# Optimization experiments

Hardware: AMD Instinct MI355X
Metric: run time of the kernel (lower is better)

Reference implementation:

```python
import jax, jax.numpy as jnp
import numpy as np

NUM_GROUPS = 32
EPS = 1e-5
HEAD_DIM = 64

def group_norm(x, w, b):
    # x: [B,C,H,W]; normalize within 32 groups over (C//32, H, W)
    B, C, H, W = x.shape
    xg = x.reshape(B, NUM_GROUPS, C // NUM_GROUPS, H, W)
    mu = xg.mean(axis=(2, 3, 4), keepdims=True)
    var = xg.var(axis=(2, 3, 4), keepdims=True)
    xn = ((xg - mu) / jnp.sqrt(var + EPS)).reshape(B, C, H, W)
    return xn * w[None, :, None, None] + b[None, :, None, None]

def conv1x1(x, w, b):
    # w: [Cout, Cin], b: [Cout]
    return jnp.einsum('bchw,oc->bohw', x, w) + b[None, :, None, None]

def setup_inputs() -> dict:
    key = jax.random.key(0)
    ks = jax.random.split(key, 12)
    B, C, Cc, H, W = 16, 512, 512, 32, 32
    s = 0.02
    return {
        'x': jax.random.normal(ks[0], (B, C, H, W), jnp.float32),
        'context': jax.random.normal(ks[1], (B, Cc, H, W), jnp.float32),
        'norm_q_w': jnp.ones((C,), jnp.float32),
        'norm_q_b': jnp.zeros((C,), jnp.float32),
        'norm_kv_w': jnp.ones((Cc,), jnp.float32),
        'norm_kv_b': jnp.zeros((Cc,), jnp.float32),
        'conv_q_w': jax.random.normal(ks[2], (C, C), jnp.float32) * s,
        'conv_q_b': jnp.zeros((C,), jnp.float32),
        'conv_kv_w': jax.random.normal(ks[3], (2 * C, Cc), jnp.float32) * s,
        'conv_kv_b': jnp.zeros((2 * C,), jnp.float32),
        'proj_w': jax.random.normal(ks[4], (C, C), jnp.float32) * s,
        'proj_b': jnp.zeros((C,), jnp.float32),
    }

def reference(x, context, norm_q_w, norm_q_b, norm_kv_w, norm_kv_b,
              conv_q_w, conv_q_b, conv_kv_w, conv_kv_b, proj_w, proj_b):
    B, C, H, W = x.shape
    nh = max(1, C // HEAD_DIM)
    hd = C // nh
    q = conv1x1(group_norm(x, norm_q_w, norm_q_b), conv_q_w, conv_q_b)
    kv = conv1x1(group_norm(context, norm_kv_w, norm_kv_b), conv_kv_w, conv_kv_b)
    k, v = jnp.split(kv, 2, axis=1)
    L = H * W
    q = q.reshape(B, nh, hd, L)
    k = k.reshape(B, nh, hd, L)
    v = v.reshape(B, nh, hd, L)
    attn = jnp.einsum('bhdi,bhdj->bhij', q, k) * (hd ** -0.5)
    attn = jax.nn.softmax(attn, axis=-1)
    out = jnp.einsum('bhij,bhdj->bhdi', attn, v)
    return x + conv1x1(out.reshape(B, C, H, W), proj_w, proj_b)
```

## Files before the change

### kernel.cpp

```cpp
#include <hip/hip_runtime.h>
#include <hip/hip_bf16.h>

typedef short v8s __attribute__((ext_vector_type(8)));
typedef float v4f __attribute__((ext_vector_type(4)));
typedef float v16f __attribute__((ext_vector_type(16)));
typedef __hip_bfloat16 bf16;

__device__ __forceinline__ float b2f(bf16 h) { return __bfloat162float(h); }
__device__ __forceinline__ bf16 f2b(float f) { return __float2bfloat16(f); }

#define QSCALE 0.18033688f

__device__ __forceinline__ void gll16(const void* g, void* l) {
    __builtin_amdgcn_global_load_lds(
        (const __attribute__((address_space(1))) void*)g,
        (__attribute__((address_space(3))) void*)l, 16, 0, 0);
}

__device__ __forceinline__ unsigned cvtpk(float lo, float hi_) {
    unsigned r;
    asm("v_cvt_pk_bf16_f32 %0, %1, %2" : "=v"(r) : "v"(lo), "v"(hi_));
    return r;
}

__device__ __forceinline__ void pl32swap(unsigned& a, unsigned& b) {
    asm("v_permlane32_swap_b32 %0, %1" : "+v"(a), "+v"(b));
}

__global__ __launch_bounds__(256) void gn_t_kernel(
    const float* __restrict__ x, const float* __restrict__ ctx,
    const float* __restrict__ qw, const float* __restrict__ qb,
    const float* __restrict__ kw, const float* __restrict__ kb,
    bf16* __restrict__ xnT, bf16* __restrict__ cnT)
{
    const int b = blockIdx.y, g = blockIdx.x, z = blockIdx.z, c0 = g * 16;
    const float* src = z ? ctx : x;
    const float* gw  = z ? kw : qw;
    const float* gb  = z ? kb : qb;
    bf16* dst = z ? cnT : xnT;
    __shared__ __attribute__((aligned(16))) bf16 lx[16][1032];
    __shared__ float rS[4], rQ[4];
    __shared__ float sSc[16], sSh[16];
    const int t = threadIdx.x, wave = t >> 6, lane = t & 63;
    const float* xb = src + ((long)b * 512 + c0) * 1024;
    float sum = 0.f, sq = 0.f;
#pragma unroll
    for (int i = 0; i < 16; i++) {
        int q = t + i * 256;
        int ci = q >> 8, l0 = (q & 255) * 4;
        float4 v = *(const float4*)(xb + (long)ci * 1024 + l0);
        sum += v.x + v.y + v.z + v.w;
        sq  += v.x * v.x + v.y * v.y + v.z * v.z + v.w * v.w;
        union { short4 s4v; bf16 h[4]; } w;
        w.h[0] = f2b(v.x); w.h[1] = f2b(v.y); w.h[2] = f2b(v.z); w.h[3] = f2b(v.w);
        *(short4*)&lx[ci][l0] = w.s4v;
    }
#pragma unroll
    for (int off = 32; off > 0; off >>= 1) {
        sum += __shfl_down(sum, off);
        sq  += __shfl_down(sq, off);
    }
    if (lane == 0) { rS[wave] = sum; rQ[wave] = sq; }
    __syncthreads();
    if (t < 16) {
        float S = rS[0] + rS[1] + rS[2] + rS[3];
        float Q = rQ[0] + rQ[1] + rQ[2] + rQ[3];
        const float inv_n = 1.f / 16384.f;
        float mean = S * inv_n;
        float var  = Q * inv_n - mean * mean;
        float rstd = rsqrtf(var + 1e-5f);
        float w = gw[c0 + t];
        sSc[t] = rstd * w;
        sSh[t] = gb[c0 + t] - mean * rstd * w;
    }
    __syncthreads();
#pragma unroll
    for (int i = 0; i < 8; i++) {
        int p = t + i * 256;
        int l = p >> 1, half = (p & 1) * 8;
        union { float4 f4; bf16 h[8]; } o_;
#pragma unroll
        for (int j = 0; j < 8; j++) {
            float y = b2f(lx[half + j][l]) * sSc[half + j] + sSh[half + j];
            o_.h[j] = f2b(y);
        }
        *(float4*)(dst + ((long)b * 1024 + l) * 512 + c0 + half) = o_.f4;
    }
}

__global__ __launch_bounds__(256) void wconv_kernel(
    const float* __restrict__ a, const float* __restrict__ bsrc,
    const float* __restrict__ csrc, bf16* __restrict__ oa,
    bf16* __restrict__ ob, bf16* __restrict__ oc)
{
    int id = blockIdx.x * 256 + threadIdx.x;
    const float* src; bf16* dst; int off;
    if (id < 65536)       { src = a;    dst = oa; off = id; }
    else if (id < 196608) { src = bsrc; dst = ob; off = id - 65536; }
    else                  { src = csrc; dst = oc; off = id - 196608; }
    float4 v = ((const float4*)src)[off];
    union { short4 s4v; bf16 h[4]; } w;
    w.h[0] = f2b(v.x); w.h[1] = f2b(v.y); w.h[2] = f2b(v.z); w.h[3] = f2b(v.w);
    ((short4*)dst)[off] = w.s4v;
}

__global__ __launch_bounds__(256) void qkv_gemm_kernel(
    const bf16* __restrict__ xnT, const bf16* __restrict__ cnT,
    const bf16* __restrict__ wQ, const bf16* __restrict__ wKV,
    bf16* __restrict__ QT, bf16* __restrict__ KT, bf16* __restrict__ Vo,
    const float* __restrict__ cqb, const float* __restrict__ ckvb)
{
    const long PB = 512L * 1024;
    const int z = blockIdx.z, op = z >> 4, bz = z & 15;
    const bf16* A; const bf16* B; bf16* C; const float* bias;
    int nBlkN, N, biasPerM; float scale;
    if (op == 0) {
        A = xnT + bz * PB; B = wQ;  C = QT + bz * PB; bias = cqb;
        nBlkN = 4; N = 512; biasPerM = 0; scale = QSCALE;
    } else if (op == 1) {
        A = cnT + bz * PB; B = wKV; C = KT + bz * PB; bias = ckvb;
        nBlkN = 4; N = 512; biasPerM = 0; scale = 1.0f;
    } else {
        A = wKV + 512L * 512; B = cnT + bz * PB; C = Vo + bz * PB; bias = ckvb + 512;
        nBlkN = 8; N = 1024; biasPerM = 1; scale = 1.0f;
    }
    const int bx = blockIdx.x;
    const int m0 = (bx / nBlkN) * 128, n0 = (bx % nBlkN) * 128;
    __shared__ __attribute__((aligned(16))) bf16 lA[128][64];
    __shared__ __attribute__((aligned(16))) bf16 lB[128][64];
    const int t = threadIdx.x, wave = t >> 6, lane = t & 63;
    const int quad = lane >> 4, c = lane & 15;
    const int wm = (wave >> 1) * 64, wn = (wave & 1) * 64;
    const int rIS = lane >> 3;
    const int chG = (lane & 7) ^ rIS;
    const bf16* Ag[4]; const bf16* Bg[4];
    bf16* Al[4]; bf16* Bl[4];
#pragma unroll
    for (int j = 0; j < 4; j++) {
        int seg = wave + j * 4;
        int row = seg * 8 + rIS;
        Ag[j] = A + (long)(m0 + row) * 512 + chG * 8;
        Bg[j] = B + (long)(n0 + row) * 512 + chG * 8;
        Al[j] = &lA[seg * 8][0];
        Bl[j] = &lB[seg * 8][0];
    }
    v4f acc[4][4] = {};
    for (int k0 = 0; k0 < 512; k0 += 64) {
        __syncthreads();
#pragma unroll
        for (int j = 0; j < 4; j++) {
            gll16(Ag[j] + k0, Al[j]);
            gll16(Bg[j] + k0, Bl[j]);
        }
        __syncthreads();
#pragma unroll
        for (int kk = 0; kk < 2; kk++) {
            v8s af[4], bfr[4];
#pragma unroll
            for (int mt = 0; mt < 4; mt++)
                af[mt] = *(const v8s*)&lA[wm + mt * 16 + c][((kk * 4 + quad) ^ (c & 7)) * 8];
#pragma unroll
            for (int nt = 0; nt < 4; nt++)
                bfr[nt] = *(const v8s*)&lB[wn + nt * 16 + c][((kk * 4 + quad) ^ (c & 7)) * 8];
#pragma unroll
            for (int mt = 0; mt < 4; mt++)
#pragma unroll
                for (int nt = 0; nt < 4; nt++)
                    acc[mt][nt] = __builtin_amdgcn_mfma_f32_16x16x32_bf16(
                        af[mt], bfr[nt], acc[mt][nt], 0, 0, 0);
        }
    }
#pragma unroll
    for (int mt = 0; mt < 4; mt++) {
#pragma unroll
        for (int nt = 0; nt < 4; nt++) {
#pragma unroll
            for (int r = 0; r < 4; r++) {
                int row = m0 + wm + mt * 16 + quad * 4 + r;
                int col = n0 + wn + nt * 16 + c;
                float v = (acc[mt][nt][r] + (biasPerM ? bias[row] : bias[col])) * scale;
                C[(long)row * N + col] = f2b(v);
            }
        }
    }
}

__global__ __launch_bounds__(256) void gemm_proj_kernel(
    const bf16* __restrict__ A,
    const bf16* __restrict__ B, long sBb,
    float* __restrict__ C,
    const float* __restrict__ bias,
    const float* __restrict__ resid,
    int M, int N)
{
    const int bz = blockIdx.z;
    const int m0 = blockIdx.x * 128, n0 = blockIdx.y * 128;
    const bf16* Bb = B + (long)bz * sBb;
    __shared__ __attribute__((aligned(16))) bf16 lA[128][64];
    __shared__ __attribute__((aligned(16))) bf16 lB[128][64];
    const int t = threadIdx.x, wave = t >> 6, lane = t & 63;
    const int quad = lane >> 4, c = lane & 15;
    const int wm = (wave >> 1) * 64, wn = (wave & 1) * 64;
    const int rIS = lane >> 3, chG = (lane & 7) ^ rIS;
    const bf16* Ag[4]; const bf16* Bg[4];
    bf16* Al[4]; bf16* Bl[4];
#pragma unroll
    for (int j = 0; j < 4; j++) {
        int seg = wave + j * 4;
        int row = seg * 8 + rIS;
        Ag[j] = A + (long)(m0 + row) * 512 + chG * 8;
        Bg[j] = Bb + (long)(n0 + row) * 512 + chG * 8;
        Al[j] = &lA[seg * 8][0];
        Bl[j] = &lB[seg * 8][0];
    }
    v4f acc[4][4] = {};
    for (int k0 = 0; k0 < 512; k0 += 64) {
        __syncthreads();
#pragma unroll
        for (int j = 0; j < 4; j++) {
            gll16(Ag[j] + k0, Al[j]);
            gll16(Bg[j] + k0, Bl[j]);
        }
        __syncthreads();
#pragma unroll
        for (int kk = 0; kk < 2; kk++) {
            v8s af[4], bfr[4];
#pragma unroll
            for (int mt = 0; mt < 4; mt++)
                af[mt] = *(const v8s*)&lA[wm + mt * 16 + c][((kk * 4 + quad) ^ (c & 7)) * 8];
#pragma unroll
            for (int nt = 0; nt < 4; nt++)
                bfr[nt] = *(const v8s*)&lB[wn + nt * 16 + c][((kk * 4 + quad) ^ (c & 7)) * 8];
#pragma unroll
            for (int mt = 0; mt < 4; mt++)
#pragma unroll
                for (int nt = 0; nt < 4; nt++)
                    acc[mt][nt] = __builtin_amdgcn_mfma_f32_16x16x32_bf16(
                        af[mt], bfr[nt], acc[mt][nt], 0, 0, 0);
        }
    }
#pragma unroll
    for (int mt = 0; mt < 4; mt++) {
#pragma unroll
        for (int nt = 0; nt < 4; nt++) {
#pragma unroll
            for (int r = 0; r < 4; r++) {
                int row = m0 + wm + mt * 16 + quad * 4 + r;
                int col = n0 + wn + nt * 16 + c;
                float v = acc[mt][nt][r] + bias[row]
                        + resid[(long)bz * ((long)M * N) + (long)row * N + col];
                C[(long)bz * ((long)M * N) + (long)row * N + col] = v;
            }
        }
    }
}

__global__ __launch_bounds__(256, 4) void attn_kernel(
    const bf16* QT, const bf16* __restrict__ KT,
    const bf16* __restrict__ V, bf16* AOT)
{
    const int nblk = blockIdx.x;
    const int s = nblk >> 3;
    const int it = s & 7;
    const int g = ((s >> 3) << 3) | (nblk & 7);
    const int h = g & 7, b = g >> 3;
    const int i0 = it * 128;
    __shared__ __attribute__((aligned(16))) bf16 lk[2][64][64];
    __shared__ __attribute__((aligned(16))) bf16 lv[2][64][64];
    const int t = threadIdx.x, wave = t >> 6, lane = t & 63;
    const int m31 = lane & 31, hi = lane >> 5;
    const int rIS = lane >> 3, chG = (lane & 7) ^ rIS;
    const bf16* Qb = QT + ((long)b * 1024 + i0 + wave * 32 + m31) * 512 + h * 64;
    v8s qf[4];
#pragma unroll
    for (int ks = 0; ks < 4; ks++)
        qf[ks] = *(const v8s*)(Qb + ks * 16 + hi * 8);
    const bf16* Kg[2]; const bf16* Vg[2];
#pragma unroll
    for (int j = 0; j < 2; j++) {
        int seg = wave * 2 + j;
        Kg[j] = KT + ((long)b * 1024 + seg * 8 + rIS) * 512 + h * 64 + chG * 8;
        Vg[j] = V + ((long)b * 512 + h * 64 + seg * 8 + rIS) * 1024 + chG * 8;
    }
#pragma unroll
    for (int j = 0; j < 2; j++) {
        int seg = wave * 2 + j;
        gll16(Kg[j], &lk[0][seg * 8][0]);
        gll16(Vg[j], &lv[0][seg * 8][0]);
    }
    float lsum = 0.f;
    v16f o0 = {}, o1 = {};

    for (int jt = 0; jt < 16; jt++) {
        const int cur = jt & 1;
        __syncthreads();
        {
            int nx = (jt + 1) & 15;
#pragma unroll
            for (int j = 0; j < 2; j++) {
                int seg = wave * 2 + j;
                gll16(Kg[j] + (long)nx * 64 * 512, &lk[1 - cur][seg * 8][0]);
                gll16(Vg[j] + (long)nx * 64, &lv[1 - cur][seg * 8][0]);
            }
        }
#pragma unroll
        for (int jb = 0; jb < 2; jb++) {
            v16f sA = {};
#pragma unroll
            for (int ks = 0; ks < 4; ks++) {
                v8s kf = *(const v8s*)&lk[cur][jb * 32 + m31][((ks * 2 + hi) ^ (m31 & 7)) * 8];
                sA = __builtin_amdgcn_mfma_f32_32x32x16_bf16(kf, qf[ks], sA, 0, 0, 0);
            }
            unsigned u[8];
#pragma unroll
            for (int k2 = 0; k2 < 8; k2++) {
                float pl = exp2f(sA[2 * k2]);
                float ph = exp2f(sA[2 * k2 + 1]);
                lsum += pl + ph;
                u[k2] = cvtpk(pl, ph);
            }
            pl32swap(u[0], u[2]); pl32swap(u[1], u[3]);
            pl32swap(u[4], u[6]); pl32swap(u[5], u[7]);
#pragma unroll
            for (int kk = 0; kk < 2; kk++) {
                union { unsigned w[4]; v8s v; } pf;
                pf.w[0] = u[4 * kk + 0]; pf.w[1] = u[4 * kk + 1];
                pf.w[2] = u[4 * kk + 2]; pf.w[3] = u[4 * kk + 3];
                const int cc2 = (jb * 2 + kk) * 2 + hi;
                v8s vf0 = *(const v8s*)&lv[cur][m31][(cc2 ^ (m31 & 7)) * 8];
                o0 = __builtin_amdgcn_mfma_f32_32x32x16_bf16(vf0, pf.v, o0, 0, 0, 0);
                v8s vf1 = *(const v8s*)&lv[cur][32 + m31][(cc2 ^ (m31 & 7)) * 8];
                o1 = __builtin_amdgcn_mfma_f32_32x32x16_bf16(vf1, pf.v, o1, 0, 0, 0);
            }
        }
    }
    float lt = lsum + __shfl_xor(lsum, 32);
    float inv = 1.f / lt;
    bf16* Ob = AOT + ((long)b * 1024 + i0 + wave * 32 + m31) * 512 + h * 64;
#pragma unroll
    for (int gq = 0; gq < 4; gq++) {
        union { short4 s4v; bf16 hh[4]; } w0, w1;
#pragma unroll
        for (int k = 0; k < 4; k++) {
            w0.hh[k] = f2b(o0[gq * 4 + k] * inv);
            w1.hh[k] = f2b(o1[gq * 4 + k] * inv);
        }
        *(short4*)(Ob + gq * 8 + hi * 4)      = w0.s4v;
        *(short4*)(Ob + 32 + gq * 8 + hi * 4) = w1.s4v;
    }
}

extern "C" void kernel_launch(void* const* d_in, const int* in_sizes, int n_in,
                              void* d_out, int out_size, void* d_ws, size_t ws_size,
                              hipStream_t stream)
{
    const float* x    = (const float*)d_in[0];
    const float* ctx  = (const float*)d_in[1];
    const float* nqw  = (const float*)d_in[2];
    const float* nqb  = (const float*)d_in[3];
    const float* nkw  = (const float*)d_in[4];
    const float* nkb  = (const float*)d_in[5];
    const float* cqw  = (const float*)d_in[6];
    const float* cqb  = (const float*)d_in[7];
    const float* ckvw = (const float*)d_in[8];
    const float* ckvb = (const float*)d_in[9];
    const float* pw   = (const float*)d_in[10];
    const float* pb   = (const float*)d_in[11];
    float* out = (float*)d_out;
    bf16* ws  = (bf16*)d_ws;

    const long PB  = 512L * 1024;
    const long TOT = 16L * PB;
    bf16* s0 = ws;
    bf16* s1 = ws + TOT;
    bf16* s2 = ws + 2 * TOT;
    bf16* s3 = ws + 3 * TOT;
    bf16* s4 = ws + 4 * TOT;
    bf16* wQ  = ws + 5 * TOT;
    bf16* wKV = wQ + 262144;
    bf16* wP  = wKV + 524288;

    dim3 blk(256);
    gn_t_kernel<<<dim3(32, 16, 2), blk, 0, stream>>>(
        x, ctx, nqw, nqb, nkw, nkb, s0, s1);
    wconv_kernel<<<dim3(1024), blk, 0, stream>>>(cqw, ckvw, pw, wQ, wKV, wP);
    qkv_gemm_kernel<<<dim3(32, 1, 48), blk, 0, stream>>>(
        s0, s1, wQ, wKV, s2, s3, s4, cqb, ckvb);
    attn_kernel<<<dim3(1024), blk, 0, stream>>>(s2, s3, s4, s2);
    gemm_proj_kernel<<<dim3(4, 8, 16), blk, 0, stream>>>(
        wP, s2, PB, out, pb, x, 512, 1024);
}
```

Baseline: 257.6 us.

## Process two query tiles per wave in attention to reuse K/V loads

```diff
diff --git a/kernel.cpp b/kernel.cpp
--- a/kernel.cpp
+++ b/kernel.cpp
@@ -255,26 +255,29 @@
     }
 }
 
-__global__ __launch_bounds__(256, 4) void attn_kernel(
+__global__ __launch_bounds__(256, 2) void attn_kernel(
     const bf16* QT, const bf16* __restrict__ KT,
     const bf16* __restrict__ V, bf16* AOT)
 {
     const int nblk = blockIdx.x;
     const int s = nblk >> 3;
-    const int it = s & 7;
-    const int g = ((s >> 3) << 3) | (nblk & 7);
+    const int it = s & 3;
+    const int g = ((s >> 2) << 3) | (nblk & 7);
     const int h = g & 7, b = g >> 3;
-    const int i0 = it * 128;
+    const int i0 = it * 256;
     __shared__ __attribute__((aligned(16))) bf16 lk[2][64][64];
     __shared__ __attribute__((aligned(16))) bf16 lv[2][64][64];
     const int t = threadIdx.x, wave = t >> 6, lane = t & 63;
     const int m31 = lane & 31, hi = lane >> 5;
     const int rIS = lane >> 3, chG = (lane & 7) ^ rIS;
-    const bf16* Qb = QT + ((long)b * 1024 + i0 + wave * 32 + m31) * 512 + h * 64;
-    v8s qf[4];
-#pragma unroll
-    for (int ks = 0; ks < 4; ks++)
-        qf[ks] = *(const v8s*)(Qb + ks * 16 + hi * 8);
+    v8s qf[2][4];
+#pragma unroll
+    for (int iq = 0; iq < 2; iq++) {
+        const bf16* Qb = QT + ((long)b * 1024 + i0 + wave * 64 + iq * 32 + m31) * 512 + h * 64;
+#pragma unroll
+        for (int ks = 0; ks < 4; ks++)
+            qf[iq][ks] = *(const v8s*)(Qb + ks * 16 + hi * 8);
+    }
     const bf16* Kg[2]; const bf16* Vg[2];
 #pragma unroll
     for (int j = 0; j < 2; j++) {
@@ -288,8 +291,8 @@
         gll16(Kg[j], &lk[0][seg * 8][0]);
         gll16(Vg[j], &lv[0][seg * 8][0]);
     }
-    float lsum = 0.f;
-    v16f o0 = {}, o1 = {};
+    float lsum[2] = {};
+    v16f o[2][2] = {};
 
     for (int jt = 0; jt < 16; jt++) {
         const int cur = jt & 1;
@@ -305,48 +308,62 @@
         }
 #pragma unroll
         for (int jb = 0; jb < 2; jb++) {
-            v16f sA = {};
+            v16f sA0 = {}, sA1 = {};
 #pragma unroll
             for (int ks = 0; ks < 4; ks++) {
                 v8s kf = *(const v8s*)&lk[cur][jb * 32 + m31][((ks * 2 + hi) ^ (m31 & 7)) * 8];
-                sA = __builtin_amdgcn_mfma_f32_32x32x16_bf16(kf, qf[ks], sA, 0, 0, 0);
-            }
-            unsigned u[8];
+                sA0 = __builtin_amdgcn_mfma_f32_32x32x16_bf16(kf, qf[0][ks], sA0, 0, 0, 0);
+                sA1 = __builtin_amdgcn_mfma_f32_32x32x16_bf16(kf, qf[1][ks], sA1, 0, 0, 0);
+            }
+            unsigned u0[8], u1[8];
 #pragma unroll
             for (int k2 = 0; k2 < 8; k2++) {
-                float pl = exp2f(sA[2 * k2]);
-                float ph = exp2f(sA[2 * k2 + 1]);
-                lsum += pl + ph;
-                u[k2] = cvtpk(pl, ph);
-            }
-            pl32swap(u[0], u[2]); pl32swap(u[1], u[3]);
-            pl32swap(u[4], u[6]); pl32swap(u[5], u[7]);
+                float p0l = exp2f(sA0[2 * k2]);
+                float p0h = exp2f(sA0[2 * k2 + 1]);
+                float p1l = exp2f(sA1[2 * k2]);
+                float p1h = exp2f(sA1[2 * k2 + 1]);
+                lsum[0] += p0l + p0h;
+                lsum[1] += p1l + p1h;
+                u0[k2] = cvtpk(p0l, p0h);
+                u1[k2] = cvtpk(p1l, p1h);
+            }
+            pl32swap(u0[0], u0[2]); pl32swap(u0[1], u0[3]);
+            pl32swap(u0[4], u0[6]); pl32swap(u0[5], u0[7]);
+            pl32swap(u1[0], u1[2]); pl32swap(u1[1], u1[3]);
+            pl32swap(u1[4], u1[6]); pl32swap(u1[5], u1[7]);
 #pragma unroll
             for (int kk = 0; kk < 2; kk++) {
-                union { unsigned w[4]; v8s v; } pf;
-                pf.w[0] = u[4 * kk + 0]; pf.w[1] = u[4 * kk + 1];
-                pf.w[2] = u[4 * kk + 2]; pf.w[3] = u[4 * kk + 3];
+                union { unsigned w[4]; v8s v; } pf0, pf1;
+                pf0.w[0] = u0[4 * kk + 0]; pf0.w[1] = u0[4 * kk + 1];
+                pf0.w[2] = u0[4 * kk + 2]; pf0.w[3] = u0[4 * kk + 3];
+                pf1.w[0] = u1[4 * kk + 0]; pf1.w[1] = u1[4 * kk + 1];
+                pf1.w[2] = u1[4 * kk + 2]; pf1.w[3] = u1[4 * kk + 3];
                 const int cc2 = (jb * 2 + kk) * 2 + hi;
                 v8s vf0 = *(const v8s*)&lv[cur][m31][(cc2 ^ (m31 & 7)) * 8];
-                o0 = __builtin_amdgcn_mfma_f32_32x32x16_bf16(vf0, pf.v, o0, 0, 0, 0);
+                o[0][0] = __builtin_amdgcn_mfma_f32_32x32x16_bf16(vf0, pf0.v, o[0][0], 0, 0, 0);
+                o[1][0] = __builtin_amdgcn_mfma_f32_32x32x16_bf16(vf0, pf1.v, o[1][0], 0, 0, 0);
                 v8s vf1 = *(const v8s*)&lv[cur][32 + m31][(cc2 ^ (m31 & 7)) * 8];
-                o1 = __builtin_amdgcn_mfma_f32_32x32x16_bf16(vf1, pf.v, o1, 0, 0, 0);
-            }
-        }
-    }
-    float lt = lsum + __shfl_xor(lsum, 32);
-    float inv = 1.f / lt;
-    bf16* Ob = AOT + ((long)b * 1024 + i0 + wave * 32 + m31) * 512 + h * 64;
-#pragma unroll
-    for (int gq = 0; gq < 4; gq++) {
-        union { short4 s4v; bf16 hh[4]; } w0, w1;
-#pragma unroll
-        for (int k = 0; k < 4; k++) {
-            w0.hh[k] = f2b(o0[gq * 4 + k] * inv);
-            w1.hh[k] = f2b(o1[gq * 4 + k] * inv);
-        }
-        *(short4*)(Ob + gq * 8 + hi * 4)      = w0.s4v;
-        *(short4*)(Ob + 32 + gq * 8 + hi * 4) = w1.s4v;
+                o[0][1] = __builtin_amdgcn_mfma_f32_32x32x16_bf16(vf1, pf0.v, o[0][1], 0, 0, 0);
+                o[1][1] = __builtin_amdgcn_mfma_f32_32x32x16_bf16(vf1, pf1.v, o[1][1], 0, 0, 0);
+            }
+        }
+    }
+#pragma unroll
+    for (int iq = 0; iq < 2; iq++) {
+        float lt = lsum[iq] + __shfl_xor(lsum[iq], 32);
+        float inv = 1.f / lt;
+        bf16* Ob = AOT + ((long)b * 1024 + i0 + wave * 64 + iq * 32 + m31) * 512 + h * 64;
+#pragma unroll
+        for (int gq = 0; gq < 4; gq++) {
+            union { short4 s4v; bf16 hh[4]; } w0, w1;
+#pragma unroll
+            for (int k = 0; k < 4; k++) {
+                w0.hh[k] = f2b(o[iq][0][gq * 4 + k] * inv);
+                w1.hh[k] = f2b(o[iq][1][gq * 4 + k] * inv);
+            }
+            *(short4*)(Ob + gq * 8 + hi * 4)      = w0.s4v;
+            *(short4*)(Ob + 32 + gq * 8 + hi * 4) = w1.s4v;
+        }
     }
 }
 
@@ -386,7 +403,7 @@
     wconv_kernel<<<dim3(1024), blk, 0, stream>>>(cqw, ckvw, pw, wQ, wKV, wP);
     qkv_gemm_kernel<<<dim3(32, 1, 48), blk, 0, stream>>>(
         s0, s1, wQ, wKV, s2, s3, s4, cqb, ckvb);
-    attn_kernel<<<dim3(1024), blk, 0, stream>>>(s2, s3, s4, s2);
+    attn_kernel<<<dim3(512), blk, 0, stream>>>(s2, s3, s4, s2);
     gemm_proj_kernel<<<dim3(4, 8, 16), blk, 0, stream>>>(
         wP, s2, PB, out, pb, x, 512, 1024);
 }
```

Measured after the change: 255.9 us. No clear change (-0.7%).
